# Performance work log

Hardware: AMD Instinct MI355X
Metric: run time of the kernel (lower is better)

The kernel has to match this reference:

```python
import jax, jax.numpy as jnp
from jax import lax
import numpy as np

B, CIN, COUT, H, W = 16, 128, 256, 64, 64
E, K, RED = 4, 3, 4

def setup_inputs() -> dict:
    key = jax.random.key(0)
    ks = jax.random.split(key, 16)
    s = 0.05
    return {
        'x': jax.random.normal(ks[0], (B, CIN, H, W), jnp.float32),
        'expert_w': jax.random.normal(ks[1], (E, COUT, CIN, K, K), jnp.float32) * s,
        'r1_w': jax.random.normal(ks[2], (E // 2, CIN), jnp.float32) * s,
        'r1_b': jnp.zeros((E // 2,), jnp.float32),
        'r2_w': jax.random.normal(ks[3], (E, E // 2), jnp.float32) * s,
        'r2_b': jnp.zeros((E,), jnp.float32),
        'r3_w': jax.random.normal(ks[4], (E, E), jnp.float32) * s,
        'r3_b': jnp.zeros((E,), jnp.float32),
        'ca1_w': jax.random.normal(ks[5], (COUT // RED, COUT), jnp.float32) * s,
        'ca1_b': jnp.zeros((COUT // RED,), jnp.float32),
        'ca2_w': jax.random.normal(ks[6], (COUT, COUT // RED), jnp.float32) * s,
        'ca2_b': jnp.zeros((COUT,), jnp.float32),
        'sa_w': jax.random.normal(ks[7], (1, COUT, 7, 7), jnp.float32) * s,
        'sa_b': jnp.zeros((1,), jnp.float32),
        'bn_gamma': jnp.ones((COUT,), jnp.float32),
        'bn_beta': jnp.zeros((COUT,), jnp.float32),
    }

def _conv(x, w, stride, pad):
    return lax.conv_general_dilated(x, w, (stride, stride), [(pad, pad), (pad, pad)],
                                     dimension_numbers=('NCHW', 'OIHW', 'NCHW'))

def reference(x, expert_w, r1_w, r1_b, r2_w, r2_b, r3_w, r3_b,
              ca1_w, ca1_b, ca2_w, ca2_b, sa_w, sa_b, bn_gamma, bn_beta):
    # --- routing: GAP -> 1x1 convs (as matmuls) -> softmax over experts ---
    g = x.mean(axis=(2, 3))                                   # [B, Cin]
    h = jax.nn.relu(g @ r1_w.T + r1_b)
    h = jax.nn.relu(h @ r2_w.T + r2_b)
    rw = jax.nn.softmax(h @ r3_w.T + r3_b, axis=1)            # [B, E]
    # --- all experts as one stacked conv, then weighted combine ---
    w = expert_w.reshape(E * COUT, CIN, K, K)
    y = _conv(x, w, 1, 1)                                     # [B, E*Cout, H, W]
    y = y.reshape(x.shape[0], E, COUT, y.shape[2], y.shape[3])
    out = jnp.einsum('be,bechw->bchw', rw, y)                 # [B, Cout, H, W]
    # --- channel attention (SE) ---
    p = out.mean(axis=(2, 3))                                  # [B, Cout]
    ca = jax.nn.sigmoid(jax.nn.relu(p @ ca1_w.T + ca1_b) @ ca2_w.T + ca2_b)
    # --- spatial attention: 7x7 conv -> sigmoid ---
    sa = jax.nn.sigmoid(_conv(out, sa_w, 1, 3) + sa_b[None, :, None, None])  # [B,1,H,W]
    out = out * ca[:, :, None, None] * sa
    # --- BatchNorm (training mode: batch statistics) + ReLU ---
    mean = out.mean(axis=(0, 2, 3))
    var = out.var(axis=(0, 2, 3))
    out = (out - mean[None, :, None, None]) * lax.rsqrt(var + 1e-5)[None, :, None, None]
    out = out * bn_gamma[None, :, None, None] + bn_beta[None, :, None, None]
    return jax.nn.relu(out)
```

## Files before the change

### kernel.cpp

```cpp
#include <hip/hip_runtime.h>
#include <math.h>

#define B_    16
#define CIN_  128
#define COUT_ 256
#define H_    64
#define W_    64
#define HW_   4096

typedef __attribute__((ext_vector_type(8))) short short8v;
typedef __attribute__((ext_vector_type(4))) float f32x4;

#define WS_GPX     0
#define WS_RW      131072
#define WS_CP      131136
#define WS_CA      196672
#define WS_PSUM    200768
#define WS_PSQ     204864
#define WS_BNSCALE 208960
#define WS_BNSHIFT 209216
#define WS_SA      209472
#define WS_WSA     275008
#define WS_WCB_F   283200
#define WS_XT_F    2642496
#define WS_U_F     WS_XT_F
#define WS_MIX_F   7103040

static __device__ __forceinline__ unsigned short f2bf(float f) {
    union { float f; unsigned int u; } v; v.f = f;
    unsigned int u = v.u;
    return (unsigned short)((u + 0x7FFFu + ((u >> 16) & 1u)) >> 16);
}
static __device__ __forceinline__ float bf2f(unsigned short h) {
    union { unsigned int u; float f; } v; v.u = ((unsigned int)h) << 16;
    return v.f;
}

__device__ __forceinline__ void gl16(const void* g, const void* l) {
    __builtin_amdgcn_global_load_lds(
        (const __attribute__((address_space(1))) unsigned int*)g,
        (__attribute__((address_space(3))) unsigned int*)l, 16, 0, 0);
}

__global__ __launch_bounds__(256) void k_xt(const float* __restrict__ x,
                                            unsigned short* __restrict__ xt,
                                            float* __restrict__ gpart) {
    int h = blockIdx.x, b = blockIdx.y;
    int t = threadIdx.x;
    int w = t & 63, c8 = t >> 6;
    unsigned short* xtb = xt + (size_t)b * 66*66*128;
    unsigned short* orow = xtb + (((size_t)(h+1))*66 + (w+1))*128;
    float* gp = gpart + ((size_t)b*64 + h)*128;
    #pragma unroll
    for (int i = 0; i < 4; ++i) {
        int ci0 = i*32 + c8*8;
        float f[8];
        short8v vv;
        #pragma unroll
        for (int j = 0; j < 8; ++j) {
            f[j] = x[(((size_t)b*CIN_ + ci0 + j)*H_ + h)*W_ + w];
            vv[j] = (short)f2bf(f[j]);
        }
        *(short8v*)(orow + ci0) = vv;
        #pragma unroll
        for (int j = 0; j < 8; ++j) {
            float s = f[j];
            s += __shfl_down(s, 32, 64);
            s += __shfl_down(s, 16, 64);
            s += __shfl_down(s, 8, 64);
            s += __shfl_down(s, 4, 64);
            s += __shfl_down(s, 2, 64);
            s += __shfl_down(s, 1, 64);
            f[j] = s;
        }
        if (w == 0) {
            #pragma unroll
            for (int j = 0; j < 8; ++j) gp[ci0 + j] = f[j];
        }
    }
    xtb[(((size_t)(h+1))*66 + (t >> 7)*65)*128 + (t & 127)] = 0;
    if (h == 0 || h == 63) {
        int r = (h == 0) ? 0 : 65;
        unsigned short* rowp = xtb + ((size_t)r*66)*128;
        for (int i = t; i < 1056; i += 256)
            *(short8v*)(rowp + (size_t)i*8) = (short8v){0,0,0,0,0,0,0,0};
    }
}

__global__ void k_route(const float* __restrict__ gpart,
                        const float* r1w, const float* r1b,
                        const float* r2w, const float* r2b,
                        const float* r3w, const float* r3b,
                        float* __restrict__ rw) {
    int b = blockIdx.x;
    int t = threadIdx.x;
    __shared__ float gl_[128];
    float s = 0.f;
    for (int h = 0; h < 64; ++h) s += gpart[((size_t)b*64 + h)*128 + t];
    gl_[t] = s * (1.f/4096.f);
    __syncthreads();
    if (t == 0) {
        float h1[2];
        for (int j = 0; j < 2; ++j) {
            float acc = r1b[j];
            for (int c = 0; c < CIN_; ++c) acc += gl_[c]*r1w[j*CIN_+c];
            h1[j] = fmaxf(acc, 0.f);
        }
        float h2[4];
        for (int e = 0; e < 4; ++e)
            h2[e] = fmaxf(r2b[e] + h1[0]*r2w[e*2] + h1[1]*r2w[e*2+1], 0.f);
        float lg[4], m = -1e30f;
        for (int e = 0; e < 4; ++e) {
            float acc = r3b[e];
            for (int j = 0; j < 4; ++j) acc += h2[j]*r3w[e*4+j];
            lg[e] = acc; m = fmaxf(m, acc);
        }
        float den = 0.f;
        for (int e = 0; e < 4; ++e) { lg[e] = expf(lg[e]-m); den += lg[e]; }
        float inv = 1.f/den;
        for (int e = 0; e < 4; ++e) rw[b*4+e] = lg[e]*inv;
    }
}

__global__ __launch_bounds__(256) void k_wcomb(const float* __restrict__ ew,
                                               const float* __restrict__ rw,
                                               unsigned short* __restrict__ wc,
                                               const float* __restrict__ saw,
                                               unsigned short* __restrict__ wsa) {
    int t = threadIdx.x;
    if (blockIdx.x >= COUT_) {
        int i = (blockIdx.x - COUT_)*256 + t;
        int tap = i >> 8, c = i & 255;
        float v = (tap < 49) ? saw[c*49 + tap] : 0.f;
        wsa[tap*256 + c] = f2bf(v);
        return;
    }
    int co = blockIdx.x;
    __shared__ float ewl[4*1152];
    __shared__ float rwl[64];
    #pragma unroll
    for (int e = 0; e < 4; ++e) {
        const float* src = ew + ((size_t)(e*COUT_ + co))*1152;
        for (int i = t; i < 1152; i += 256) ewl[e*1152 + i] = src[i];
    }
    if (t < 64) rwl[t] = rw[t];
    __syncthreads();
    for (int i = 0; i < 72; ++i) {
        int f = i*256 + t;
        int b = f / 1152;
        int rem = f - b*1152;
        int tap = rem >> 7, ci = rem & 127;
        int lidx = ci*9 + tap;
        float v = rwl[b*4+0]*ewl[0*1152+lidx] + rwl[b*4+1]*ewl[1*1152+lidx]
                + rwl[b*4+2]*ewl[2*1152+lidx] + rwl[b*4+3]*ewl[3*1152+lidx];
        wc[((size_t)(b*9 + tap)*COUT_ + co)*128 + ci] = f2bf(v);
    }
}

__global__ __launch_bounds__(256) void k_conv(const unsigned short* __restrict__ xt,
                                              const unsigned short* __restrict__ wc,
                                              unsigned short* __restrict__ mixb,
                                              float* __restrict__ cpart) {
    __shared__ unsigned short xs[1600*8];
    __shared__ unsigned short wl[2304*8];
    __shared__ float gsl[4][64];
    int ht = blockIdx.x;
    int cb = blockIdx.y;
    int b  = blockIdx.z;
    int t  = threadIdx.x;
    int wv = t >> 6, lane = t & 63;
    int lr = lane & 15, kq = lane >> 4;
    int h0 = ht * 4;

    const unsigned short* xtb = xt + (size_t)b * 66*66*128;
    const unsigned short* wcb = wc + (size_t)b * 9*256*128;

    f32x4 acc[4][4];
    #pragma unroll
    for (int m = 0; m < 4; ++m)
        #pragma unroll
        for (int n = 0; n < 4; ++n) acc[m][n] = (f32x4){0.f,0.f,0.f,0.f};

    for (int ci0 = 0; ci0 < CIN_; ci0 += 32) {
        __syncthreads();
        for (int j = wv; j < 25; j += 4) {
            int s = j*64 + lane;
            if (s > 1583) s = 1583;
            int pos = s >> 2, q = s & 3;
            int rp = pos / 66, cp = pos - rp*66;
            const unsigned short* g = xtb + (((size_t)(h0 + rp)*66 + cp)*128 + ci0 + q*8);
            gl16(g, (const char*)xs + (size_t)j*1024);
        }
        for (int j = wv; j < 36; j += 4) {
            int s = j*64 + lane;
            int tap = s >> 8, col = (s >> 2) & 63, q = s & 3;
            const unsigned short* g = wcb + (((size_t)tap*COUT_ + cb*64 + col)*128 + ci0 + q*8);
            gl16(g, (const char*)wl + (size_t)j*1024);
        }
        asm volatile("s_waitcnt vmcnt(0)" ::: "memory");
        __syncthreads();

        #pragma unroll
        for (int dh = 0; dh < 3; ++dh) {
            #pragma unroll
            for (int dw = 0; dw < 3; ++dw) {
                int tap = dh*3 + dw;
                short8v af[4], bfv[4];
                #pragma unroll
                for (int m = 0; m < 4; ++m)
                    af[m] = *(const short8v*)(wl + ((size_t)tap*2048 + (m*16 + lr)*32 + kq*8));
                #pragma unroll
                for (int n = 0; n < 4; ++n)
                    bfv[n] = *(const short8v*)(xs + ((size_t)(wv+dh)*2112 + (n*16 + lr + dw)*32 + kq*8));
                #pragma unroll
                for (int m = 0; m < 4; ++m)
                    #pragma unroll
                    for (int n = 0; n < 4; ++n)
                        acc[m][n] = __builtin_amdgcn_mfma_f32_16x16x32_bf16(
                            af[m], bfv[n], acc[m][n], 0, 0, 0);
            }
        }
    }

    unsigned short* ob = mixb + ((size_t)b*COUT_ + cb*64)*HW_ + (h0 + wv)*W_;
    #pragma unroll
    for (int m = 0; m < 4; ++m)
        #pragma unroll
        for (int n = 0; n < 4; ++n) {
            f32x4 v = acc[m][n];
            #pragma unroll
            for (int r = 0; r < 4; ++r)
                ob[(size_t)(m*16 + kq*4 + r)*HW_ + n*16 + lr] = f2bf(v[r]);
        }

    float gp[4][4];
    #pragma unroll
    for (int m = 0; m < 4; ++m)
        #pragma unroll
        for (int r = 0; r < 4; ++r)
            gp[m][r] = acc[m][0][r] + acc[m][1][r] + acc[m][2][r] + acc[m][3][r];
    #pragma unroll
    for (int o = 8; o > 0; o >>= 1)
        #pragma unroll
        for (int m = 0; m < 4; ++m)
            #pragma unroll
            for (int r = 0; r < 4; ++r)
                gp[m][r] += __shfl_down(gp[m][r], o, 64);
    if ((lane & 15) == 0) {
        #pragma unroll
        for (int m = 0; m < 4; ++m)
            #pragma unroll
            for (int r = 0; r < 4; ++r)
                gsl[wv][m*16 + kq*4 + r] = gp[m][r];
    }
    __syncthreads();
    if (t < 64) {
        float s = gsl[0][t] + gsl[1][t] + gsl[2][t] + gsl[3][t];
        cpart[((size_t)b*16 + ht)*COUT_ + cb*64 + t] = s;
    }
}

__global__ void k_ca(const float* __restrict__ cpart, const float* ca1w, const float* ca1b,
                     const float* ca2w, const float* ca2b, float* __restrict__ ca) {
    int b = blockIdx.x;
    int t = threadIdx.x;
    __shared__ float pfull[256];
    __shared__ float h1[64];
    for (int i = t; i < 256; i += 64) {
        float s = 0.f;
        for (int h = 0; h < 16; ++h) s += cpart[((size_t)b*16 + h)*COUT_ + i];
        pfull[i] = s * (1.f/(float)HW_);
    }
    __syncthreads();
    float s = ca1b[t];
    for (int c = 0; c < COUT_; ++c) s += pfull[c] * ca1w[t*COUT_ + c];
    h1[t] = fmaxf(s, 0.f);
    __syncthreads();
    for (int i = 0; i < 4; ++i) {
        int co = t*4 + i;
        float s2 = ca2b[co];
        for (int j = 0; j < 64; ++j) s2 += h1[j] * ca2w[co*64 + j];
        ca[b*COUT_ + co] = 1.f/(1.f + expf(-s2));
    }
}

__global__ __launch_bounds__(256) void k_sa_gemm(const unsigned short* __restrict__ mixb,
                                                 const unsigned short* __restrict__ wsa,
                                                 float* __restrict__ u) {
    __shared__ unsigned short wl[16384];
    __shared__ unsigned short bt[16384];
    int pxt = blockIdx.x;
    int b   = blockIdx.y;
    int t = threadIdx.x, wv = t >> 6, lane = t & 63;
    int lr = lane & 15, kq = lane >> 4;
    int px0 = pxt * 64;

    #pragma unroll
    for (int k = 0; k < 8; ++k) {
        int s = t + k*256;
        int row = s >> 5, cs = s & 31;
        short8v v = *(const short8v*)(wsa + row*256 + cs*8);
        int off = row*512 + ((cs*16) ^ ((row & 7) << 4));
        *(short8v*)((char*)wl + off) = v;
    }
    {
        int px = lane;
        const unsigned short* mb = mixb + (size_t)b*COUT_*HW_ + px0 + px;
        #pragma unroll
        for (int c8 = 0; c8 < 8; ++c8) {
            int cb = wv*64 + c8*8;
            short8v v;
            #pragma unroll
            for (int j = 0; j < 8; ++j)
                v[j] = (short)mb[(size_t)(cb + j)*HW_];
            int off = px*512 + ((cb*2) ^ ((px & 7) << 4));
            *(short8v*)((char*)bt + off) = v;
        }
    }
    __syncthreads();

    f32x4 acc[4];
    #pragma unroll
    for (int n = 0; n < 4; ++n) acc[n] = (f32x4){0.f,0.f,0.f,0.f};

    #pragma unroll
    for (int ks = 0; ks < 8; ++ks) {
        int ci0 = ks*32;
        int arow = wv*16 + lr;
        short8v a = *(const short8v*)((const char*)wl +
                        arow*512 + (((ci0 + kq*8)*2) ^ ((arow & 7) << 4)));
        #pragma unroll
        for (int n = 0; n < 4; ++n) {
            int prow = n*16 + lr;
            short8v bv = *(const short8v*)((const char*)bt +
                            prow*512 + (((ci0 + kq*8)*2) ^ ((prow & 7) << 4)));
            acc[n] = __builtin_amdgcn_mfma_f32_16x16x32_bf16(a, bv, acc[n], 0, 0, 0);
        }
    }

    float* ub = u + (size_t)b*64*HW_;
    #pragma unroll
    for (int n = 0; n < 4; ++n)
        #pragma unroll
        for (int r = 0; r < 4; ++r)
            ub[(size_t)(wv*16 + kq*4 + r)*HW_ + px0 + n*16 + lr] = acc[n][r];
}

__global__ void k_sared(const float* __restrict__ u, const float* __restrict__ sab,
                        float* __restrict__ sa) {
    int b = blockIdx.y;
    int h = blockIdx.x * 4 + (threadIdx.x >> 6);
    int w = threadIdx.x & 63;
    float s = sab[0];
    const float* ub = u + (size_t)b*64*HW_;
    #pragma unroll
    for (int dh = 0; dh < 7; ++dh) {
        int hh = h + dh - 3;
        if (hh < 0 || hh >= H_) continue;
        #pragma unroll
        for (int dw = 0; dw < 7; ++dw) {
            int ww = w + dw - 3;
            if (ww < 0 || ww >= W_) continue;
            s += ub[(size_t)(dh*7 + dw)*HW_ + hh*W_ + ww];
        }
    }
    sa[(size_t)b*HW_ + h*W_ + w] = 1.f/(1.f + expf(-s));
}

__global__ void k_stats(const unsigned short* __restrict__ mixb, const float* __restrict__ ca,
                        const float* __restrict__ sa,
                        float* __restrict__ psum, float* __restrict__ psq) {
    int c = blockIdx.x & 255;
    int b = blockIdx.x >> 8;
    float cav = ca[b*COUT_ + c];
    const unsigned short* pl = mixb + ((size_t)b*COUT_ + c) * HW_;
    const float* sab = sa + (size_t)b * HW_;
    float s = 0.f, sq = 0.f;
    for (int i = threadIdx.x; i < HW_/8; i += 256) {
        short8v v = ((const short8v*)pl)[i];
        float4 w0 = ((const float4*)sab)[2*i];
        float4 w1 = ((const float4*)sab)[2*i+1];
        float f0 = bf2f((unsigned short)v[0])*cav*w0.x;
        float f1 = bf2f((unsigned short)v[1])*cav*w0.y;
        float f2 = bf2f((unsigned short)v[2])*cav*w0.z;
        float f3 = bf2f((unsigned short)v[3])*cav*w0.w;
        float f4 = bf2f((unsigned short)v[4])*cav*w1.x;
        float f5 = bf2f((unsigned short)v[5])*cav*w1.y;
        float f6 = bf2f((unsigned short)v[6])*cav*w1.z;
        float f7 = bf2f((unsigned short)v[7])*cav*w1.w;
        s  += f0+f1+f2+f3+f4+f5+f6+f7;
        sq += f0*f0+f1*f1+f2*f2+f3*f3+f4*f4+f5*f5+f6*f6+f7*f7;
    }
    for (int o = 32; o > 0; o >>= 1) { s += __shfl_down(s,o,64); sq += __shfl_down(sq,o,64); }
    __shared__ float ls[8];
    int wid = threadIdx.x>>6, lane = threadIdx.x&63;
    if (lane==0) { ls[wid]=s; ls[4+wid]=sq; }
    __syncthreads();
    if (threadIdx.x==0) {
        psum[b*COUT_+c] = ls[0]+ls[1]+ls[2]+ls[3];
        psq [b*COUT_+c] = ls[4]+ls[5]+ls[6]+ls[7];
    }
}

__global__ void k_bnfin(const float* __restrict__ psum, const float* __restrict__ psq,
                        const float* __restrict__ gamma, const float* __restrict__ beta,
                        float* __restrict__ scale, float* __restrict__ shift) {
    int c = threadIdx.x;
    float s=0.f, q=0.f;
    for (int b = 0; b < B_; ++b) { s += psum[b*COUT_+c]; q += psq[b*COUT_+c]; }
    float n = (float)(B_*HW_);
    float mean = s/n;
    float var = q/n - mean*mean;
    float sc = gamma[c] * rsqrtf(var + 1e-5f);
    scale[c] = sc;
    shift[c] = beta[c] - mean*sc;
}

__global__ void k_bnapply(const unsigned short* __restrict__ mixb, float* __restrict__ out,
                          const float* __restrict__ ca, const float* __restrict__ sa,
                          const float* __restrict__ scale, const float* __restrict__ shift) {
    size_t i = (size_t)blockIdx.x * 256 + threadIdx.x;
    int c = (int)((i >> 9) & 255);
    int b = (int)(i >> 17);
    int px8 = (int)(i & 511);
    float cav = ca[b*COUT_ + c];
    float sc = scale[c], sh = shift[c];
    short8v v = ((const short8v*)mixb)[i];
    const float4* sp = (const float4*)(sa + (size_t)b*HW_) + (size_t)px8*2;
    float4 w0 = sp[0], w1 = sp[1];
    float4 o0, o1;
    o0.x = fmaxf(fmaf(bf2f((unsigned short)v[0])*cav*w0.x, sc, sh), 0.f);
    o0.y = fmaxf(fmaf(bf2f((unsigned short)v[1])*cav*w0.y, sc, sh), 0.f);
    o0.z = fmaxf(fmaf(bf2f((unsigned short)v[2])*cav*w0.z, sc, sh), 0.f);
    o0.w = fmaxf(fmaf(bf2f((unsigned short)v[3])*cav*w0.w, sc, sh), 0.f);
    o1.x = fmaxf(fmaf(bf2f((unsigned short)v[4])*cav*w1.x, sc, sh), 0.f);
    o1.y = fmaxf(fmaf(bf2f((unsigned short)v[5])*cav*w1.y, sc, sh), 0.f);
    o1.z = fmaxf(fmaf(bf2f((unsigned short)v[6])*cav*w1.z, sc, sh), 0.f);
    o1.w = fmaxf(fmaf(bf2f((unsigned short)v[7])*cav*w1.w, sc, sh), 0.f);
    ((float4*)out)[i*2]   = o0;
    ((float4*)out)[i*2+1] = o1;
}

extern "C" void kernel_launch(void* const* d_in, const int* in_sizes, int n_in,
                              void* d_out, int out_size, void* d_ws, size_t ws_size,
                              hipStream_t stream) {
    const float* x    = (const float*)d_in[0];
    const float* ew   = (const float*)d_in[1];
    const float* r1w  = (const float*)d_in[2];
    const float* r1b  = (const float*)d_in[3];
    const float* r2w  = (const float*)d_in[4];
    const float* r2b  = (const float*)d_in[5];
    const float* r3w  = (const float*)d_in[6];
    const float* r3b  = (const float*)d_in[7];
    const float* ca1w = (const float*)d_in[8];
    const float* ca1b = (const float*)d_in[9];
    const float* ca2w = (const float*)d_in[10];
    const float* ca2b = (const float*)d_in[11];
    const float* saw  = (const float*)d_in[12];
    const float* sab  = (const float*)d_in[13];
    const float* gm   = (const float*)d_in[14];
    const float* bt   = (const float*)d_in[15];
    float* out = (float*)d_out;
    float* ws  = (float*)d_ws;
    unsigned short* wcb  = (unsigned short*)(ws + WS_WCB_F);
    unsigned short* xt   = (unsigned short*)(ws + WS_XT_F);
    unsigned short* wsa  = (unsigned short*)(ws + WS_WSA);
    unsigned short* mixb = (unsigned short*)(ws + WS_MIX_F);
    float* u = ws + WS_U_F;

    k_xt<<<dim3(64,16), 256, 0, stream>>>(x, xt, ws+WS_GPX);
    k_route<<<16, 128, 0, stream>>>(ws+WS_GPX, r1w, r1b, r2w, r2b, r3w, r3b, ws+WS_RW);
    k_wcomb<<<320, 256, 0, stream>>>(ew, ws+WS_RW, wcb, saw, wsa);
    k_conv<<<dim3(16,4,16), 256, 0, stream>>>(xt, wcb, mixb, ws+WS_CP);
    k_ca<<<B_, 64, 0, stream>>>(ws+WS_CP, ca1w, ca1b, ca2w, ca2b, ws+WS_CA);
    k_sa_gemm<<<dim3(64,16), 256, 0, stream>>>(mixb, wsa, u);
    k_sared<<<dim3(16,16), 256, 0, stream>>>(u, sab, ws+WS_SA);
    k_stats<<<B_*COUT_, 256, 0, stream>>>(mixb, ws+WS_CA, ws+WS_SA, ws+WS_PSUM, ws+WS_PSQ);
    k_bnfin<<<1, 256, 0, stream>>>(ws+WS_PSUM, ws+WS_PSQ, gm, bt, ws+WS_BNSCALE, ws+WS_BNSHIFT);
    k_bnapply<<<8192, 256, 0, stream>>>(mixb, out, ws+WS_CA, ws+WS_SA, ws+WS_BNSCALE, ws+WS_BNSHIFT);
}
```

Before: 152.3 us.

## Retile conv to one output row per block with register-streamed weights

The conv kernel now computes one output row for all 256 output channels per block, with each wave owning 64 channels. Weights are re-laid out by ci-quarter so each wave loads its A fragments straight from global memory into registers, double-buffered across taps, instead of staging them in LDS. The output tile is transposed through swizzled LDS so mixb gets 16-byte coalesced stores. Channel partial sums now have 64 row entries per batch, so the workspace offsets and the k_ca reduction grow. This trades higher global weight traffic (only L2 reuse) for less LDS staging and better store coalescing.

```diff
diff --git a/kernel.cpp b/kernel.cpp
--- a/kernel.cpp
+++ b/kernel.cpp
@@ -14,17 +14,17 @@
 #define WS_GPX     0
 #define WS_RW      131072
 #define WS_CP      131136
-#define WS_CA      196672
-#define WS_PSUM    200768
-#define WS_PSQ     204864
-#define WS_BNSCALE 208960
-#define WS_BNSHIFT 209216
-#define WS_SA      209472
-#define WS_WSA     275008
-#define WS_WCB_F   283200
-#define WS_XT_F    2642496
+#define WS_CA      393280
+#define WS_PSUM    397376
+#define WS_PSQ     401472
+#define WS_BNSCALE 405568
+#define WS_BNSHIFT 405824
+#define WS_SA      406080
+#define WS_WSA     471616
+#define WS_WCB_F   479808
+#define WS_XT_F    2839104
 #define WS_U_F     WS_XT_F
-#define WS_MIX_F   7103040
+#define WS_MIX_F   7299648
 
 static __device__ __forceinline__ unsigned short f2bf(float f) {
     union { float f; unsigned int u; } v; v.f = f;
@@ -153,7 +153,7 @@
         int lidx = ci*9 + tap;
         float v = rwl[b*4+0]*ewl[0*1152+lidx] + rwl[b*4+1]*ewl[1*1152+lidx]
                 + rwl[b*4+2]*ewl[2*1152+lidx] + rwl[b*4+3]*ewl[3*1152+lidx];
-        wc[((size_t)(b*9 + tap)*COUT_ + co)*128 + ci] = f2bf(v);
+        wc[(((size_t)(b*9 + tap)*4 + (ci >> 5))*COUT_ + co)*32 + (ci & 31)] = f2bf(v);
     }
 }
 
@@ -161,19 +161,17 @@
                                               const unsigned short* __restrict__ wc,
                                               unsigned short* __restrict__ mixb,
                                               float* __restrict__ cpart) {
-    __shared__ unsigned short xs[1600*8];
-    __shared__ unsigned short wl[2304*8];
-    __shared__ float gsl[4][64];
-    int ht = blockIdx.x;
-    int cb = blockIdx.y;
-    int b  = blockIdx.z;
-    int t  = threadIdx.x;
+    __shared__ __align__(16) unsigned short xs[3*66*32];
+    __shared__ __align__(16) unsigned short ts[256*64];
+    int h = blockIdx.x;
+    int b = blockIdx.y;
+    int t = threadIdx.x;
     int wv = t >> 6, lane = t & 63;
     int lr = lane & 15, kq = lane >> 4;
-    int h0 = ht * 4;
-
-    const unsigned short* xtb = xt + (size_t)b * 66*66*128;
-    const unsigned short* wcb = wc + (size_t)b * 9*256*128;
+
+    const unsigned short* xtb = xt + ((size_t)b*66 + h)*66*128;
+    const unsigned short* wlb = wc + (size_t)b*9*4*256*32
+                                   + (size_t)(wv*64 + lr)*32 + kq*8;
 
     f32x4 acc[4][4];
     #pragma unroll
@@ -181,82 +179,87 @@
         #pragma unroll
         for (int n = 0; n < 4; ++n) acc[m][n] = (f32x4){0.f,0.f,0.f,0.f};
 
-    for (int ci0 = 0; ci0 < CIN_; ci0 += 32) {
+    for (int ciq = 0; ciq < 4; ++ciq) {
         __syncthreads();
-        for (int j = wv; j < 25; j += 4) {
+        for (int j = wv; j < 13; j += 4) {
             int s = j*64 + lane;
-            if (s > 1583) s = 1583;
-            int pos = s >> 2, q = s & 3;
-            int rp = pos / 66, cp = pos - rp*66;
-            const unsigned short* g = xtb + (((size_t)(h0 + rp)*66 + cp)*128 + ci0 + q*8);
-            gl16(g, (const char*)xs + (size_t)j*1024);
-        }
-        for (int j = wv; j < 36; j += 4) {
-            int s = j*64 + lane;
-            int tap = s >> 8, col = (s >> 2) & 63, q = s & 3;
-            const unsigned short* g = wcb + (((size_t)tap*COUT_ + cb*64 + col)*128 + ci0 + q*8);
-            gl16(g, (const char*)wl + (size_t)j*1024);
-        }
+            if (s < 792) {
+                int pos = s >> 2, q = s & 3;
+                gl16(xtb + (size_t)pos*128 + ciq*32 + q*8, (const char*)xs + (size_t)j*1024);
+            }
+        }
+        short8v af[2][4];
+        #pragma unroll
+        for (int m = 0; m < 4; ++m)
+            af[0][m] = *(const short8v*)(wlb + ((size_t)(0*4 + ciq)*256 + m*16)*32);
         asm volatile("s_waitcnt vmcnt(0)" ::: "memory");
         __syncthreads();
 
         #pragma unroll
-        for (int dh = 0; dh < 3; ++dh) {
-            #pragma unroll
-            for (int dw = 0; dw < 3; ++dw) {
-                int tap = dh*3 + dw;
-                short8v af[4], bfv[4];
+        for (int tap = 0; tap < 9; ++tap) {
+            if (tap < 8) {
                 #pragma unroll
                 for (int m = 0; m < 4; ++m)
-                    af[m] = *(const short8v*)(wl + ((size_t)tap*2048 + (m*16 + lr)*32 + kq*8));
+                    af[(tap+1)&1][m] =
+                        *(const short8v*)(wlb + ((size_t)((tap+1)*4 + ciq)*256 + m*16)*32);
+            }
+            short8v bf[4];
+            #pragma unroll
+            for (int n = 0; n < 4; ++n)
+                bf[n] = *(const short8v*)(xs +
+                           ((size_t)((tap/3)*66 + n*16 + lr + (tap%3))*32 + kq*8));
+            #pragma unroll
+            for (int m = 0; m < 4; ++m)
                 #pragma unroll
                 for (int n = 0; n < 4; ++n)
-                    bfv[n] = *(const short8v*)(xs + ((size_t)(wv+dh)*2112 + (n*16 + lr + dw)*32 + kq*8));
+                    acc[m][n] = __builtin_amdgcn_mfma_f32_16x16x32_bf16(
+                        af[tap&1][m], bf[n], acc[m][n], 0, 0, 0);
+        }
+    }
+
+    {
+        float gp[4][4];
+        #pragma unroll
+        for (int m = 0; m < 4; ++m)
+            #pragma unroll
+            for (int r = 0; r < 4; ++r)
+                gp[m][r] = acc[m][0][r] + acc[m][1][r] + acc[m][2][r] + acc[m][3][r];
+        #pragma unroll
+        for (int o = 1; o < 16; o <<= 1)
+            #pragma unroll
+            for (int m = 0; m < 4; ++m)
                 #pragma unroll
-                for (int m = 0; m < 4; ++m)
-                    #pragma unroll
-                    for (int n = 0; n < 4; ++n)
-                        acc[m][n] = __builtin_amdgcn_mfma_f32_16x16x32_bf16(
-                            af[m], bfv[n], acc[m][n], 0, 0, 0);
+                for (int r = 0; r < 4; ++r)
+                    gp[m][r] += __shfl_xor(gp[m][r], o, 64);
+        if (lr == 0) {
+            #pragma unroll
+            for (int m = 0; m < 4; ++m)
+                #pragma unroll
+                for (int r = 0; r < 4; ++r)
+                    cpart[((size_t)b*64 + h)*256 + wv*64 + m*16 + kq*4 + r] = gp[m][r];
+        }
+    }
+
+    #pragma unroll
+    for (int m = 0; m < 4; ++m)
+        #pragma unroll
+        for (int n = 0; n < 4; ++n)
+            #pragma unroll
+            for (int r = 0; r < 4; ++r) {
+                int co_l = wv*64 + m*16 + kq*4 + r;
+                int px = n*16 + lr;
+                int off = (co_l*128 + px*2) ^ ((co_l & 7) << 4);
+                *(unsigned short*)((char*)ts + off) = f2bf(acc[m][n][r]);
             }
-        }
-    }
-
-    unsigned short* ob = mixb + ((size_t)b*COUT_ + cb*64)*HW_ + (h0 + wv)*W_;
-    #pragma unroll
-    for (int m = 0; m < 4; ++m)
-        #pragma unroll
-        for (int n = 0; n < 4; ++n) {
-            f32x4 v = acc[m][n];
-            #pragma unroll
-            for (int r = 0; r < 4; ++r)
-                ob[(size_t)(m*16 + kq*4 + r)*HW_ + n*16 + lr] = f2bf(v[r]);
-        }
-
-    float gp[4][4];
-    #pragma unroll
-    for (int m = 0; m < 4; ++m)
-        #pragma unroll
-        for (int r = 0; r < 4; ++r)
-            gp[m][r] = acc[m][0][r] + acc[m][1][r] + acc[m][2][r] + acc[m][3][r];
-    #pragma unroll
-    for (int o = 8; o > 0; o >>= 1)
-        #pragma unroll
-        for (int m = 0; m < 4; ++m)
-            #pragma unroll
-            for (int r = 0; r < 4; ++r)
-                gp[m][r] += __shfl_down(gp[m][r], o, 64);
-    if ((lane & 15) == 0) {
-        #pragma unroll
-        for (int m = 0; m < 4; ++m)
-            #pragma unroll
-            for (int r = 0; r < 4; ++r)
-                gsl[wv][m*16 + kq*4 + r] = gp[m][r];
-    }
-    __syncthreads();
-    if (t < 64) {
-        float s = gsl[0][t] + gsl[1][t] + gsl[2][t] + gsl[3][t];
-        cpart[((size_t)b*16 + ht)*COUT_ + cb*64 + t] = s;
+    __syncthreads();
+    unsigned short* ob = mixb + ((size_t)b*COUT_)*HW_ + h*64;
+    #pragma unroll
+    for (int c = 0; c < 8; ++c) {
+        int k = c*256 + t;
+        int co = k >> 3, c16 = k & 7;
+        int off = (co*128 + c16*16) ^ ((co & 7) << 4);
+        short8v v = *(const short8v*)((const char*)ts + off);
+        *(short8v*)(ob + (size_t)co*HW_ + c16*8) = v;
     }
 }
 
@@ -268,7 +271,7 @@
     __shared__ float h1[64];
     for (int i = t; i < 256; i += 64) {
         float s = 0.f;
-        for (int h = 0; h < 16; ++h) s += cpart[((size_t)b*16 + h)*COUT_ + i];
+        for (int h = 0; h < 64; ++h) s += cpart[((size_t)b*64 + h)*256 + i];
         pfull[i] = s * (1.f/(float)HW_);
     }
     __syncthreads();
@@ -471,7 +474,7 @@
     k_xt<<<dim3(64,16), 256, 0, stream>>>(x, xt, ws+WS_GPX);
     k_route<<<16, 128, 0, stream>>>(ws+WS_GPX, r1w, r1b, r2w, r2b, r3w, r3b, ws+WS_RW);
     k_wcomb<<<320, 256, 0, stream>>>(ew, ws+WS_RW, wcb, saw, wsa);
-    k_conv<<<dim3(16,4,16), 256, 0, stream>>>(xt, wcb, mixb, ws+WS_CP);
+    k_conv<<<dim3(64,16), 256, 0, stream>>>(xt, wcb, mixb, ws+WS_CP);
     k_ca<<<B_, 64, 0, stream>>>(ws+WS_CP, ca1w, ca1b, ca2w, ca2b, ws+WS_CA);
     k_sa_gemm<<<dim3(64,16), 256, 0, stream>>>(mixb, wsa, u);
     k_sared<<<dim3(16,16), 256, 0, stream>>>(u, sab, ws+WS_SA);
```

New measurement: 178.7 us. 1.17x slower.

## Fuse SE/spatial-attention and BN stats kernels, remap workgroups across XCDs

Applied to the files above, without the earlier changes.

Merges the channel-attention MLP into the spatial-attention reduction kernel and the BN stats plus finalize into one per-channel kernel, cutting three launches. It also remaps workgroup IDs in several kernels so consecutive logical tiles land on the same XCD, aiming at better L2 locality. The stats kernel now uses only 256 blocks, each looping over 16 batches, which lowers parallelism for that reduction.

```diff
diff --git a/kernel.cpp b/kernel.cpp
--- a/kernel.cpp
+++ b/kernel.cpp
@@ -15,8 +15,6 @@
 #define WS_RW      131072
 #define WS_CP      131136
 #define WS_CA      196672
-#define WS_PSUM    200768
-#define WS_PSQ     204864
 #define WS_BNSCALE 208960
 #define WS_BNSHIFT 209216
 #define WS_SA      209472
@@ -45,7 +43,9 @@
 __global__ __launch_bounds__(256) void k_xt(const float* __restrict__ x,
                                             unsigned short* __restrict__ xt,
                                             float* __restrict__ gpart) {
-    int h = blockIdx.x, b = blockIdx.y;
+    int wg = blockIdx.x + (blockIdx.y << 6);
+    int nw = ((wg & 7) << 7) + (wg >> 3);
+    int h = nw & 63, b = nw >> 6;
     int t = threadIdx.x;
     int w = t & 63, c8 = t >> 6;
     unsigned short* xtb = xt + (size_t)b * 66*66*128;
@@ -164,9 +164,11 @@
     __shared__ unsigned short xs[1600*8];
     __shared__ unsigned short wl[2304*8];
     __shared__ float gsl[4][64];
-    int ht = blockIdx.x;
-    int cb = blockIdx.y;
-    int b  = blockIdx.z;
+    int wg = blockIdx.x + (blockIdx.y << 4) + (blockIdx.z << 6);
+    int nw = ((wg & 7) << 7) + (wg >> 3);
+    int ht = nw & 15;
+    int cb = (nw >> 4) & 3;
+    int b  = nw >> 6;
     int t  = threadIdx.x;
     int wv = t >> 6, lane = t & 63;
     int lr = lane & 15, kq = lane >> 4;
@@ -260,37 +262,15 @@
     }
 }
 
-__global__ void k_ca(const float* __restrict__ cpart, const float* ca1w, const float* ca1b,
-                     const float* ca2w, const float* ca2b, float* __restrict__ ca) {
-    int b = blockIdx.x;
-    int t = threadIdx.x;
-    __shared__ float pfull[256];
-    __shared__ float h1[64];
-    for (int i = t; i < 256; i += 64) {
-        float s = 0.f;
-        for (int h = 0; h < 16; ++h) s += cpart[((size_t)b*16 + h)*COUT_ + i];
-        pfull[i] = s * (1.f/(float)HW_);
-    }
-    __syncthreads();
-    float s = ca1b[t];
-    for (int c = 0; c < COUT_; ++c) s += pfull[c] * ca1w[t*COUT_ + c];
-    h1[t] = fmaxf(s, 0.f);
-    __syncthreads();
-    for (int i = 0; i < 4; ++i) {
-        int co = t*4 + i;
-        float s2 = ca2b[co];
-        for (int j = 0; j < 64; ++j) s2 += h1[j] * ca2w[co*64 + j];
-        ca[b*COUT_ + co] = 1.f/(1.f + expf(-s2));
-    }
-}
-
 __global__ __launch_bounds__(256) void k_sa_gemm(const unsigned short* __restrict__ mixb,
                                                  const unsigned short* __restrict__ wsa,
                                                  float* __restrict__ u) {
     __shared__ unsigned short wl[16384];
     __shared__ unsigned short bt[16384];
-    int pxt = blockIdx.x;
-    int b   = blockIdx.y;
+    int wg = blockIdx.x + (blockIdx.y << 6);
+    int nw = ((wg & 7) << 7) + (wg >> 3);
+    int pxt = nw & 63;
+    int b   = nw >> 6;
     int t = threadIdx.x, wv = t >> 6, lane = t & 63;
     int lr = lane & 15, kq = lane >> 4;
     int px0 = pxt * 64;
@@ -346,80 +326,104 @@
             ub[(size_t)(wv*16 + kq*4 + r)*HW_ + px0 + n*16 + lr] = acc[n][r];
 }
 
-__global__ void k_sared(const float* __restrict__ u, const float* __restrict__ sab,
-                        float* __restrict__ sa) {
-    int b = blockIdx.y;
-    int h = blockIdx.x * 4 + (threadIdx.x >> 6);
-    int w = threadIdx.x & 63;
-    float s = sab[0];
-    const float* ub = u + (size_t)b*64*HW_;
-    #pragma unroll
-    for (int dh = 0; dh < 7; ++dh) {
-        int hh = h + dh - 3;
-        if (hh < 0 || hh >= H_) continue;
-        #pragma unroll
-        for (int dw = 0; dw < 7; ++dw) {
-            int ww = w + dw - 3;
-            if (ww < 0 || ww >= W_) continue;
-            s += ub[(size_t)(dh*7 + dw)*HW_ + hh*W_ + ww];
-        }
-    }
-    sa[(size_t)b*HW_ + h*W_ + w] = 1.f/(1.f + expf(-s));
-}
-
-__global__ void k_stats(const unsigned short* __restrict__ mixb, const float* __restrict__ ca,
-                        const float* __restrict__ sa,
-                        float* __restrict__ psum, float* __restrict__ psq) {
-    int c = blockIdx.x & 255;
-    int b = blockIdx.x >> 8;
-    float cav = ca[b*COUT_ + c];
-    const unsigned short* pl = mixb + ((size_t)b*COUT_ + c) * HW_;
-    const float* sab = sa + (size_t)b * HW_;
+__global__ void k_sared_ca(const float* __restrict__ u, const float* __restrict__ sab,
+                           float* __restrict__ sa,
+                           const float* __restrict__ cpart,
+                           const float* __restrict__ ca1w, const float* __restrict__ ca1b,
+                           const float* __restrict__ ca2w, const float* __restrict__ ca2b,
+                           float* __restrict__ ca) {
+    int wg = blockIdx.x + (blockIdx.y << 4);
+    int nw = ((wg & 7) << 5) + (wg >> 3);
+    int hg = nw & 15;
+    int b  = nw >> 4;
+    int t = threadIdx.x;
+    {
+        int h = hg * 4 + (t >> 6);
+        int w = t & 63;
+        float s = sab[0];
+        const float* ub = u + (size_t)b*64*HW_;
+        #pragma unroll
+        for (int dh = 0; dh < 7; ++dh) {
+            int hh = h + dh - 3;
+            if (hh < 0 || hh >= H_) continue;
+            #pragma unroll
+            for (int dw = 0; dw < 7; ++dw) {
+                int ww = w + dw - 3;
+                if (ww < 0 || ww >= W_) continue;
+                s += ub[(size_t)(dh*7 + dw)*HW_ + hh*W_ + ww];
+            }
+        }
+        sa[(size_t)b*HW_ + h*W_ + w] = 1.f/(1.f + expf(-s));
+    }
+    if (hg == 0) {
+        __shared__ float pfull[256];
+        __shared__ float h1[64];
+        float s0 = 0.f;
+        for (int h = 0; h < 16; ++h) s0 += cpart[((size_t)b*16 + h)*COUT_ + t];
+        pfull[t] = s0 * (1.f/(float)HW_);
+        __syncthreads();
+        if (t < 64) {
+            float s = ca1b[t];
+            for (int c = 0; c < COUT_; ++c) s += pfull[c] * ca1w[t*COUT_ + c];
+            h1[t] = fmaxf(s, 0.f);
+        }
+        __syncthreads();
+        float s2 = ca2b[t];
+        for (int j = 0; j < 64; ++j) s2 += h1[j] * ca2w[t*64 + j];
+        ca[b*COUT_ + t] = 1.f/(1.f + expf(-s2));
+    }
+}
+
+__global__ void k_statsfin(const unsigned short* __restrict__ mixb,
+                           const float* __restrict__ ca, const float* __restrict__ sa,
+                           const float* __restrict__ gamma, const float* __restrict__ beta,
+                           float* __restrict__ scale, float* __restrict__ shift) {
+    int c = blockIdx.x;
+    int t = threadIdx.x;
     float s = 0.f, sq = 0.f;
-    for (int i = threadIdx.x; i < HW_/8; i += 256) {
-        short8v v = ((const short8v*)pl)[i];
-        float4 w0 = ((const float4*)sab)[2*i];
-        float4 w1 = ((const float4*)sab)[2*i+1];
-        float f0 = bf2f((unsigned short)v[0])*cav*w0.x;
-        float f1 = bf2f((unsigned short)v[1])*cav*w0.y;
-        float f2 = bf2f((unsigned short)v[2])*cav*w0.z;
-        float f3 = bf2f((unsigned short)v[3])*cav*w0.w;
-        float f4 = bf2f((unsigned short)v[4])*cav*w1.x;
-        float f5 = bf2f((unsigned short)v[5])*cav*w1.y;
-        float f6 = bf2f((unsigned short)v[6])*cav*w1.z;
-        float f7 = bf2f((unsigned short)v[7])*cav*w1.w;
-        s  += f0+f1+f2+f3+f4+f5+f6+f7;
-        sq += f0*f0+f1*f1+f2*f2+f3*f3+f4*f4+f5*f5+f6*f6+f7*f7;
+    for (int b = 0; b < B_; ++b) {
+        float cav = ca[b*COUT_ + c];
+        const unsigned short* pl = mixb + ((size_t)b*COUT_ + c) * HW_;
+        const float* sab = sa + (size_t)b * HW_;
+        for (int i = t; i < HW_/8; i += 256) {
+            short8v v = ((const short8v*)pl)[i];
+            float4 w0 = ((const float4*)sab)[2*i];
+            float4 w1 = ((const float4*)sab)[2*i+1];
+            float f0 = bf2f((unsigned short)v[0])*cav*w0.x;
+            float f1 = bf2f((unsigned short)v[1])*cav*w0.y;
+            float f2 = bf2f((unsigned short)v[2])*cav*w0.z;
+            float f3 = bf2f((unsigned short)v[3])*cav*w0.w;
+            float f4 = bf2f((unsigned short)v[4])*cav*w1.x;
+            float f5 = bf2f((unsigned short)v[5])*cav*w1.y;
+            float f6 = bf2f((unsigned short)v[6])*cav*w1.z;
+            float f7 = bf2f((unsigned short)v[7])*cav*w1.w;
+            s  += f0+f1+f2+f3+f4+f5+f6+f7;
+            sq += f0*f0+f1*f1+f2*f2+f3*f3+f4*f4+f5*f5+f6*f6+f7*f7;
+        }
     }
     for (int o = 32; o > 0; o >>= 1) { s += __shfl_down(s,o,64); sq += __shfl_down(sq,o,64); }
     __shared__ float ls[8];
-    int wid = threadIdx.x>>6, lane = threadIdx.x&63;
-    if (lane==0) { ls[wid]=s; ls[4+wid]=sq; }
+    int wid = t >> 6, lane = t & 63;
+    if (lane == 0) { ls[wid] = s; ls[4+wid] = sq; }
     __syncthreads();
-    if (threadIdx.x==0) {
-        psum[b*COUT_+c] = ls[0]+ls[1]+ls[2]+ls[3];
-        psq [b*COUT_+c] = ls[4]+ls[5]+ls[6]+ls[7];
-    }
-}
-
-__global__ void k_bnfin(const float* __restrict__ psum, const float* __restrict__ psq,
-                        const float* __restrict__ gamma, const float* __restrict__ beta,
-                        float* __restrict__ scale, float* __restrict__ shift) {
-    int c = threadIdx.x;
-    float s=0.f, q=0.f;
-    for (int b = 0; b < B_; ++b) { s += psum[b*COUT_+c]; q += psq[b*COUT_+c]; }
-    float n = (float)(B_*HW_);
-    float mean = s/n;
-    float var = q/n - mean*mean;
-    float sc = gamma[c] * rsqrtf(var + 1e-5f);
-    scale[c] = sc;
-    shift[c] = beta[c] - mean*sc;
+    if (t == 0) {
+        float ts = ls[0]+ls[1]+ls[2]+ls[3];
+        float tq = ls[4]+ls[5]+ls[6]+ls[7];
+        float n = (float)(B_*HW_);
+        float mean = ts/n;
+        float var = tq/n - mean*mean;
+        float sc = gamma[c] * rsqrtf(var + 1e-5f);
+        scale[c] = sc;
+        shift[c] = beta[c] - mean*sc;
+    }
 }
 
 __global__ void k_bnapply(const unsigned short* __restrict__ mixb, float* __restrict__ out,
                           const float* __restrict__ ca, const float* __restrict__ sa,
                           const float* __restrict__ scale, const float* __restrict__ shift) {
-    size_t i = (size_t)blockIdx.x * 256 + threadIdx.x;
+    int wg = blockIdx.x;
+    int nw = ((wg & 7) << 10) + (wg >> 3);
+    size_t i = (size_t)nw * 256 + threadIdx.x;
     int c = (int)((i >> 9) & 255);
     int b = (int)(i >> 17);
     int px8 = (int)(i & 511);
@@ -472,10 +476,11 @@
     k_route<<<16, 128, 0, stream>>>(ws+WS_GPX, r1w, r1b, r2w, r2b, r3w, r3b, ws+WS_RW);
     k_wcomb<<<320, 256, 0, stream>>>(ew, ws+WS_RW, wcb, saw, wsa);
     k_conv<<<dim3(16,4,16), 256, 0, stream>>>(xt, wcb, mixb, ws+WS_CP);
-    k_ca<<<B_, 64, 0, stream>>>(ws+WS_CP, ca1w, ca1b, ca2w, ca2b, ws+WS_CA);
     k_sa_gemm<<<dim3(64,16), 256, 0, stream>>>(mixb, wsa, u);
-    k_sared<<<dim3(16,16), 256, 0, stream>>>(u, sab, ws+WS_SA);
-    k_stats<<<B_*COUT_, 256, 0, stream>>>(mixb, ws+WS_CA, ws+WS_SA, ws+WS_PSUM, ws+WS_PSQ);
-    k_bnfin<<<1, 256, 0, stream>>>(ws+WS_PSUM, ws+WS_PSQ, gm, bt, ws+WS_BNSCALE, ws+WS_BNSHIFT);
-    k_bnapply<<<8192, 256, 0, stream>>>(mixb, out, ws+WS_CA, ws+WS_SA, ws+WS_BNSCALE, ws+WS_BNSHIFT);
-}
+    k_sared_ca<<<dim3(16,16), 256, 0, stream>>>(u, sab, ws+WS_SA, ws+WS_CP,
+                                                ca1w, ca1b, ca2w, ca2b, ws+WS_CA);
+    k_statsfin<<<256, 256, 0, stream>>>(mixb, ws+WS_CA, ws+WS_SA, gm, bt,
+                                        ws+WS_BNSCALE, ws+WS_BNSHIFT);
+    k_bnapply<<<8192, 256, 0, stream>>>(mixb, out, ws+WS_CA, ws+WS_SA,
+                                        ws+WS_BNSCALE, ws+WS_BNSHIFT);
+}
```

Result: faster. 143.3 us (-5.9%).
